# Optimization experiments

Measured on AMD Instinct MI355X. Metric: run time of the kernel, lower is better.

Reference implementation:

```python
import jax, jax.numpy as jnp
import numpy as np
import math

N_HEADS = 8

def _head_dirs():
    # 8 trigrams = corners of {-1,+1}^3, L2-normalized -> each row / sqrt(3)
    t = np.array([[ (i >> 2 & 1) * 2 - 1, (i >> 1 & 1) * 2 - 1, (i & 1) * 2 - 1]
                  for i in range(8)], dtype=np.float32)
    return jnp.asarray(t / np.sqrt(3.0, dtype=np.float32))

def setup_inputs() -> dict:
    key = jax.random.key(0)
    k1, k2, k3, k4 = jax.random.split(key, 4)
    B, T, C = 2, 2048, 1024
    x = jax.random.normal(k1, (B, T, C), dtype=jnp.float32)
    w_qkv = jax.random.normal(k2, (C, 3 * C), dtype=jnp.float32) * (1.0 / math.sqrt(C))
    w_out = jax.random.normal(k3, (C, C), dtype=jnp.float32) * (1.0 / math.sqrt(C))
    head_scales = jax.random.normal(k4, (N_HEADS,), dtype=jnp.float32) * 0.1
    return {"x": x, "w_qkv": w_qkv, "w_out": w_out, "head_scales": head_scales}

def reference(x, w_qkv, w_out, head_scales):
    B, T, C = x.shape
    H = N_HEADS
    hd = C // H
    scale = 1.0 / math.sqrt(hd)
    dirs = _head_dirs()  # [H,3], fixed buffer

    qkv = (x @ w_qkv).reshape(B, T, 3, H, hd)
    q = jnp.transpose(qkv[:, :, 0], (0, 2, 1, 3))  # [B,H,T,hd]
    k = jnp.transpose(qkv[:, :, 1], (0, 2, 1, 3))
    v = jnp.transpose(qkv[:, :, 2], (0, 2, 1, 3))

    scores = jnp.einsum('bhqd,bhkd->bhqk', q, k) * scale  # [B,H,T,T]
    causal = jnp.tril(jnp.ones((T, T), dtype=bool))
    scores = jnp.where(causal[None, None], scores, -jnp.inf)

    # rank-1 geometric (trigram) bias on first 3 dims of q,k
    q_proj = jnp.einsum('bhtd,hd->bht', q[..., :3], dirs)  # [B,H,T]
    k_proj = jnp.einsum('bhtd,hd->bht', k[..., :3], dirs)
    geo = q_proj[..., :, None] * k_proj[..., None, :]       # [B,H,T,T]
    scores = scores + head_scales[None, :, None, None] * geo

    attn = jax.nn.softmax(scores, axis=-1)
    out = jnp.einsum('bhqk,bhkd->bqhd', attn, v).reshape(B, T, C)
    return out @ w_out
```

## Files before the change

### kernel.cpp

```cpp
#include <hip/hip_runtime.h>
#include <hip/hip_bf16.h>
#include <cstdint>
#include <cstddef>


namespace {
constexpr int kB = 2, kT = 2048, kC = 1024, kHD = 128;
constexpr int kM = kB * kT;
constexpr int kN3 = 3 * kC;
constexpr float kScale = 0.08838834764831845f;
constexpr float kInvS3 = 0.57735026918962576f;
constexpr float kL2E  = 1.4426950408889634f;
}

typedef __bf16 bf16x8 __attribute__((ext_vector_type(8)));
typedef float f32x4 __attribute__((ext_vector_type(4)));
typedef unsigned short u16x8 __attribute__((ext_vector_type(8)));
typedef unsigned short u16x4 __attribute__((ext_vector_type(4)));
typedef unsigned int u32x4 __attribute__((ext_vector_type(4)));

__device__ __forceinline__ unsigned short f2b(float f) {
  return __builtin_bit_cast(unsigned short, (__bf16)f);
}
__device__ __forceinline__ float b2f(unsigned short u) {
  return (float)__builtin_bit_cast(__bf16, u);
}
__device__ __forceinline__ void gll16(const void* g, void* lds) {
  __builtin_amdgcn_global_load_lds(
      (const __attribute__((address_space(1))) unsigned int*)g,
      (__attribute__((address_space(3))) unsigned int*)lds, 16, 0, 0);
}
__device__ __forceinline__ bf16x8 ldsv(const unsigned short* p) {
  return __builtin_bit_cast(bf16x8, *(const u16x8*)p);
}

__global__ void k_cvt(const float* __restrict__ in, unsigned short* __restrict__ out, int n4) {
  int i = blockIdx.x * 256 + threadIdx.x;
  if (i >= n4) return;
  float4 v = ((const float4*)in)[i];
  u16x4 o = { f2b(v.x), f2b(v.y), f2b(v.z), f2b(v.w) };
  ((u16x4*)out)[i] = o;
}

__global__ void k_tc(const float* __restrict__ in, unsigned short* __restrict__ out,
                     int R, int Cin) {
  __shared__ float tile[64][65];
  const int t = threadIdx.x;
  const int r0 = blockIdx.y * 64, c0 = blockIdx.x * 64;
  const int tr = t >> 4, tc4 = (t & 15) * 4;
#pragma unroll
  for (int rr = 0; rr < 4; ++rr) {
    int r = tr + rr * 16;
    float4 v = *(const float4*)&in[(size_t)(r0 + r) * Cin + c0 + tc4];
    tile[r][tc4 + 0] = v.x; tile[r][tc4 + 1] = v.y;
    tile[r][tc4 + 2] = v.z; tile[r][tc4 + 3] = v.w;
  }
  __syncthreads();
#pragma unroll
  for (int rr = 0; rr < 4; ++rr) {
    int c = tr + rr * 16;
    u16x4 o = { f2b(tile[tc4 + 0][c]), f2b(tile[tc4 + 1][c]),
                f2b(tile[tc4 + 2][c]), f2b(tile[tc4 + 3][c]) };
    *(u16x4*)&out[(size_t)(c0 + c) * R + r0 + tc4] = o;
  }
}

__global__ __launch_bounds__(256, 2) void k_gemm(
    const unsigned short* __restrict__ A,
    const unsigned short* __restrict__ Bt,
    unsigned short* __restrict__ Cb,
    float* __restrict__ Cf,
    int M, int N, int K, int ldc) {
  __shared__ unsigned short sA[2][4096];
  __shared__ unsigned short sB[2][4096];
  const int t = threadIdx.x;
  const int lane = t & 63, wave = t >> 6;
  const int g = lane >> 4, c16 = lane & 15;
  const int wr = wave >> 1, wc = wave & 1;
  const int brow = blockIdx.x * 128, bcol = blockIdx.y * 128;
  const int NT = K >> 5;

  f32x4 acc[4][4];
#pragma unroll
  for (int m = 0; m < 4; ++m)
#pragma unroll
    for (int n = 0; n < 4; ++n) acc[m][n] = 0.f;

  auto stage = [&](int buf, int kt) {
    const int k0 = kt * 32;
#pragma unroll
    for (int is = 0; is < 2; ++is) {
      int row = is * 64 + (t >> 2);
      int gs = (t & 3) ^ (row & 3);
      gll16(&A[(size_t)(brow + row) * K + k0 + gs * 8], &sA[buf][is * 2048 + wave * 512]);
      gll16(&Bt[(size_t)(bcol + row) * K + k0 + gs * 8], &sB[buf][is * 2048 + wave * 512]);
    }
  };

  stage(0, 0);
  __syncthreads();
  for (int kt = 0; kt < NT; ++kt) {
    if (kt + 1 < NT) stage((kt + 1) & 1, kt + 1);
    const int buf = kt & 1;
    bf16x8 av[4], bv[4];
#pragma unroll
    for (int m = 0; m < 4; ++m) {
      int row = wr * 64 + m * 16 + c16;
      av[m] = ldsv(&sA[buf][row * 32 + (g ^ (row & 3)) * 8]);
    }
#pragma unroll
    for (int n = 0; n < 4; ++n) {
      int row = wc * 64 + n * 16 + c16;
      bv[n] = ldsv(&sB[buf][row * 32 + (g ^ (row & 3)) * 8]);
    }
    __builtin_amdgcn_s_setprio(1);
#pragma unroll
    for (int m = 0; m < 4; ++m)
#pragma unroll
      for (int n = 0; n < 4; ++n)
        acc[m][n] = __builtin_amdgcn_mfma_f32_16x16x32_bf16(av[m], bv[n], acc[m][n], 0, 0, 0);
    __builtin_amdgcn_s_setprio(0);
    __syncthreads();
  }

  const int orow = brow + wr * 64, ocol = bcol + wc * 64;
  if (Cb != nullptr) {
#pragma unroll
    for (int m = 0; m < 4; ++m)
#pragma unroll
      for (int n = 0; n < 4; ++n)
#pragma unroll
        for (int jj = 0; jj < 4; ++jj)
          Cb[(size_t)(orow + m * 16 + g * 4 + jj) * ldc + ocol + n * 16 + c16] =
              f2b(acc[m][n][jj]);
  } else {
#pragma unroll
    for (int m = 0; m < 4; ++m)
#pragma unroll
      for (int n = 0; n < 4; ++n)
#pragma unroll
        for (int jj = 0; jj < 4; ++jj)
          Cf[(size_t)(orow + m * 16 + g * 4 + jj) * ldc + ocol + n * 16 + c16] =
              acc[m][n][jj];
  }
}

__constant__ unsigned char kItem[44] = {
  60, 61,
  62, 56, 57, 58, 52,
  53, 54, 48, 49,
  50, 44, 45, 46, 40,
  41, 42, 36, 37,
  38, 32, 33, 34, 28,
  29, 30, 24, 25,
  26, 20, 21, 22, 16,
  17, 18, 12, 13, 8, 9,
  14, 4, 5, 0 };

__global__ __launch_bounds__(256, 2) void k_attn(
    const unsigned short* __restrict__ qkv,
    const float* __restrict__ head_scales,
    unsigned short* __restrict__ pO0,
    unsigned short* __restrict__ pO1,
    unsigned short* __restrict__ pO2,
    float2* __restrict__ pml) {
  __shared__ unsigned short sK[2][8192];
  __shared__ unsigned short sVt[2][128 * 72];
  __shared__ float sKp[2][64];

  const int t = threadIdx.x;
  const int lane = t & 63, wave = t >> 6;
  const int g = lane >> 4, c16 = lane & 15;
  const int bh = blockIdx.x;
  const int it = kItem[blockIdx.y];
  const int qt = it >> 2, c = it & 3;
  const int n = 2 * qt + 2;
  const int nc = (qt == 0) ? 1 : (qt <= 2) ? 2 : 3;
  const int cbase = n / nc, crem = n % nc;
  const int t0 = c * cbase + (c < crem ? c : crem);
  const int t1 = t0 + cbase + (c < crem ? 1 : 0);

  const int b = bh >> 3, h = bh & 7;
  const float hs = head_scales[h];
  const float sx = (h & 4) ? 1.f : -1.f;
  const float sy = (h & 2) ? 1.f : -1.f;
  const float sz = (h & 1) ? 1.f : -1.f;

  const int q0w = qt * 128 + wave * 32;
  const size_t rowbase = (size_t)b * kT;

  bf16x8 aq[2][4];
  float qp[2];
#pragma unroll
  for (int m = 0; m < 2; ++m) {
    const unsigned short* qrow = &qkv[(rowbase + q0w + m * 16 + c16) * kN3 + h * kHD];
#pragma unroll
    for (int ks = 0; ks < 4; ++ks) aq[m][ks] = ldsv(qrow + ks * 32 + g * 8);
    qp[m] = hs * kInvS3 * (sx * b2f(qrow[0]) + sy * b2f(qrow[1]) + sz * b2f(qrow[2]));
  }

  float mrow[2] = { -__builtin_inff(), -__builtin_inff() };
  float lrow[2] = { 0.f, 0.f };
  f32x4 oacc[2][8];
#pragma unroll
  for (int m = 0; m < 2; ++m)
#pragma unroll
    for (int dn = 0; dn < 8; ++dn) oacc[m][dn] = 0.f;

  uint4 vr[4];
  uint2 kpr;

  auto stageK = [&](int jt, int buf) {
    const int j0 = jt * 64;
#pragma unroll
    for (int is = 0; is < 4; ++is) {
      int row = is * 16 + (t >> 4);
      int gp = t & 15;
      int gs = (gp & 8) | ((gp ^ (row & 7)) & 7);
      gll16(&qkv[(rowbase + j0 + row) * kN3 + kC + h * kHD + gs * 8],
            &sK[buf][is * 2048 + wave * 512]);
    }
  };
  auto loadV = [&](int jt) {
#pragma unroll
    for (int itr = 0; itr < 4; ++itr)
      vr[itr] = *(const uint4*)&qkv[(rowbase + jt * 64 + lane) * kN3 + 2 * kC + h * kHD
                                    + (itr * 4 + wave) * 8];
  };
  auto writeV = [&](int buf) {
    unsigned int* sVtw = (unsigned int*)&sVt[buf][0];
    const int odd = lane & 1, pr = lane >> 1;
#pragma unroll
    for (int itr = 0; itr < 4; ++itr) {
      const int dg = itr * 4 + wave;
      uint4 my = vr[itr];
      unsigned int nx = __shfl_xor(my.x, 1), ny = __shfl_xor(my.y, 1);
      unsigned int nz = __shfl_xor(my.z, 1), nw = __shfl_xor(my.w, 1);
      unsigned int m01 = odd ? my.z : my.x, m23 = odd ? my.w : my.y;
      unsigned int n01 = odd ? nz : nx,     n23 = odd ? nw : ny;
      const int eb = odd * 4;
      unsigned int me, ne, w;
      me = m01 & 0xffffu;  ne = n01 & 0xffffu;
      w = odd ? (ne | (me << 16)) : (me | (ne << 16));
      sVtw[(dg * 8 + eb + 0) * 36 + pr] = w;
      me = m01 >> 16;      ne = n01 >> 16;
      w = odd ? (ne | (me << 16)) : (me | (ne << 16));
      sVtw[(dg * 8 + eb + 1) * 36 + pr] = w;
      me = m23 & 0xffffu;  ne = n23 & 0xffffu;
      w = odd ? (ne | (me << 16)) : (me | (ne << 16));
      sVtw[(dg * 8 + eb + 2) * 36 + pr] = w;
      me = m23 >> 16;      ne = n23 >> 16;
      w = odd ? (ne | (me << 16)) : (me | (ne << 16));
      sVtw[(dg * 8 + eb + 3) * 36 + pr] = w;
    }
  };
  auto loadKp = [&](int jt) {
    if (wave == 0)
      kpr = *(const uint2*)&qkv[(rowbase + jt * 64 + lane) * kN3 + kC + h * kHD];
  };
  auto writeKp = [&](int buf) {
    if (wave == 0) {
      float e0 = b2f((unsigned short)(kpr.x & 0xffffu));
      float e1 = b2f((unsigned short)(kpr.x >> 16));
      float e2 = b2f((unsigned short)(kpr.y & 0xffffu));
      sKp[buf][lane] = kInvS3 * (sx * e0 + sy * e1 + sz * e2);
    }
  };

  stageK(t0, 0); loadV(t0); loadKp(t0);
  writeV(0); writeKp(0);
  __syncthreads();

  for (int jt = t0; jt < t1; ++jt) {
    const int buf = (jt - t0) & 1;
    const bool more = (jt + 1 < t1);
    if (more) { stageK(jt + 1, buf ^ 1); loadV(jt + 1); loadKp(jt + 1); }

    const int j0 = jt * 64;
    f32x4 s[2][4];
#pragma unroll
    for (int m = 0; m < 2; ++m)
#pragma unroll
      for (int nn = 0; nn < 4; ++nn) s[m][nn] = 0.f;
#pragma unroll
    for (int ks = 0; ks < 4; ++ks) {
      bf16x8 kb[4];
#pragma unroll
      for (int nn = 0; nn < 4; ++nn) {
        int gp = ks * 4 + g;
        int gp2 = (gp & 8) | ((gp ^ (c16 & 7)) & 7);
        kb[nn] = ldsv(&sK[buf][(nn * 16 + c16) * 128 + gp2 * 8]);
      }
      __builtin_amdgcn_s_setprio(1);
#pragma unroll
      for (int m = 0; m < 2; ++m)
#pragma unroll
        for (int nn = 0; nn < 4; ++nn)
          s[m][nn] = __builtin_amdgcn_mfma_f32_16x16x32_bf16(kb[nn], aq[m][ks], s[m][nn], 0, 0, 0);
      __builtin_amdgcn_s_setprio(0);
    }

    float kpv[4][4];
#pragma unroll
    for (int nn = 0; nn < 4; ++nn)
#pragma unroll
      for (int jj = 0; jj < 4; ++jj) kpv[nn][jj] = sKp[buf][nn * 16 + g * 4 + jj];

    const bool edge = (jt >= 2 * qt);
    unsigned int paf[2][2][4];
#pragma unroll
    for (int m = 0; m < 2; ++m) {
      const int qg = q0w + m * 16 + c16;
      float vmax = -__builtin_inff();
#pragma unroll
      for (int nn = 0; nn < 4; ++nn)
#pragma unroll
        for (int jj = 0; jj < 4; ++jj) {
          float xv = s[m][nn][jj] * kScale + qp[m] * kpv[nn][jj];
          if (edge) {
            int kvg = j0 + nn * 16 + g * 4 + jj;
            xv = (kvg <= qg) ? xv : -__builtin_inff();
          }
          s[m][nn][jj] = xv;
          vmax = fmaxf(vmax, xv);
        }
      vmax = fmaxf(vmax, __shfl_xor(vmax, 16, 64));
      vmax = fmaxf(vmax, __shfl_xor(vmax, 32, 64));

      if (__any(vmax > mrow[m] + 8.f)) {
        float mnew = fmaxf(mrow[m], vmax);
        float mc0 = fmaxf(mnew, -1e30f);
        float alpha = exp2f((mrow[m] - mc0) * kL2E);
        mrow[m] = mnew;
        lrow[m] *= alpha;
        float ao[4];
#pragma unroll
        for (int jj = 0; jj < 4; ++jj)
          ao[jj] = __shfl(alpha, (lane & 48) | (g * 4 + jj), 64);
#pragma unroll
        for (int dn = 0; dn < 8; ++dn)
#pragma unroll
          for (int jj = 0; jj < 4; ++jj) oacc[m][dn][jj] *= ao[jj];
      }

      unsigned int pk[4][2];
      {
        const float mc = fmaxf(mrow[m], -1e30f);
        float ls = 0.f;
#pragma unroll
        for (int nn = 0; nn < 4; ++nn) {
          float p0 = exp2f((s[m][nn][0] - mc) * kL2E);
          float p1 = exp2f((s[m][nn][1] - mc) * kL2E);
          float p2 = exp2f((s[m][nn][2] - mc) * kL2E);
          float p3 = exp2f((s[m][nn][3] - mc) * kL2E);
          ls += (p0 + p1) + (p2 + p3);
          pk[nn][0] = (unsigned)f2b(p0) | ((unsigned)f2b(p1) << 16);
          pk[nn][1] = (unsigned)f2b(p2) | ((unsigned)f2b(p3) << 16);
        }
        lrow[m] += ls;
      }
#pragma unroll
      for (int ks2 = 0; ks2 < 2; ++ks2)
#pragma unroll
        for (int w = 0; w < 4; ++w) {
          int src = c16 + (((lane >> 4) & 1) * 2 + (w >> 1)) * 16;
          int va  = __shfl((int)pk[2 * ks2][w & 1], src, 64);
          int vb_ = __shfl((int)pk[2 * ks2 + 1][w & 1], src, 64);
          paf[m][ks2][w] = (unsigned)((lane & 32) ? vb_ : va);
        }
    }

#pragma unroll
    for (int ks2 = 0; ks2 < 2; ++ks2) {
      bf16x8 pa0 = __builtin_bit_cast(bf16x8,
          (u32x4){paf[0][ks2][0], paf[0][ks2][1], paf[0][ks2][2], paf[0][ks2][3]});
      bf16x8 pa1 = __builtin_bit_cast(bf16x8,
          (u32x4){paf[1][ks2][0], paf[1][ks2][1], paf[1][ks2][2], paf[1][ks2][3]});
      __builtin_amdgcn_s_setprio(1);
#pragma unroll
      for (int dn = 0; dn < 8; ++dn) {
        bf16x8 vb = ldsv(&sVt[buf][(dn * 16 + c16) * 72 + ks2 * 32 + g * 8]);
        oacc[0][dn] = __builtin_amdgcn_mfma_f32_16x16x32_bf16(pa0, vb, oacc[0][dn], 0, 0, 0);
        oacc[1][dn] = __builtin_amdgcn_mfma_f32_16x16x32_bf16(pa1, vb, oacc[1][dn], 0, 0, 0);
      }
      __builtin_amdgcn_s_setprio(0);
    }

    if (more) { writeV(buf ^ 1); writeKp(buf ^ 1); }
    __syncthreads();
  }

  unsigned short* pout = (c == 0) ? pO0 : (c == 1) ? pO1 : pO2;
#pragma unroll
  for (int m = 0; m < 2; ++m) {
    float lt = lrow[m];
    lt += __shfl_xor(lt, 16, 64);
    lt += __shfl_xor(lt, 32, 64);
    if (g == 0) {
      int rowi = wave * 32 + m * 16 + c16;
      pml[c * 32768 + (bh * 16 + qt) * 128 + rowi] = make_float2(mrow[m], lt);
    }
#pragma unroll
    for (int dn = 0; dn < 8; ++dn)
#pragma unroll
      for (int jj = 0; jj < 4; ++jj) {
        int r = q0w + m * 16 + g * 4 + jj;
        pout[(rowbase + r) * kC + h * kHD + dn * 16 + c16] = f2b(oacc[m][dn][jj]);
      }
  }
}

__global__ void k_comb(unsigned short* __restrict__ p0,
                       const unsigned short* __restrict__ p1,
                       const unsigned short* __restrict__ p2,
                       const float2* __restrict__ pml) {
  const int bh = blockIdx.x, qt = blockIdx.y;
  const int t = threadIdx.x;
  const int row = t >> 1, half = t & 1;
  const int b = bh >> 3, h = bh & 7;
  const size_t base = ((size_t)b * kT + qt * 128 + row) * kC + h * kHD + half * 64;
  const int nc = (qt == 0) ? 1 : (qt <= 2) ? 2 : 3;
  const int mli = (bh * 16 + qt) * 128 + row;
  float2 ml0 = pml[mli];
  float2 ml1 = make_float2(-1e30f, 0.f), ml2 = make_float2(-1e30f, 0.f);
  float mm = ml0.x;
  if (nc > 1) { ml1 = pml[32768 + mli]; mm = fmaxf(mm, ml1.x); }
  if (nc > 2) { ml2 = pml[65536 + mli]; mm = fmaxf(mm, ml2.x); }
  const float w0 = exp2f((ml0.x - mm) * kL2E);
  const float w1 = (nc > 1) ? exp2f((ml1.x - mm) * kL2E) : 0.f;
  const float w2 = (nc > 2) ? exp2f((ml2.x - mm) * kL2E) : 0.f;
  const float inv = 1.0f / (w0 * ml0.y + w1 * ml1.y + w2 * ml2.y);
#pragma unroll
  for (int i = 0; i < 8; ++i) {
    u16x8 o0 = *(const u16x8*)&p0[base + i * 8];
    u16x8 r;
    if (nc == 1) {
#pragma unroll
      for (int j = 0; j < 8; ++j) r[j] = f2b(b2f(o0[j]) * inv);
    } else if (nc == 2) {
      u16x8 o1 = *(const u16x8*)&p1[base + i * 8];
#pragma unroll
      for (int j = 0; j < 8; ++j)
        r[j] = f2b((w0 * b2f(o0[j]) + w1 * b2f(o1[j])) * inv);
    } else {
      u16x8 o1 = *(const u16x8*)&p1[base + i * 8];
      u16x8 o2 = *(const u16x8*)&p2[base + i * 8];
#pragma unroll
      for (int j = 0; j < 8; ++j)
        r[j] = f2b((w0 * b2f(o0[j]) + w1 * b2f(o1[j]) + w2 * b2f(o2[j])) * inv);
    }
    *(u16x8*)&p0[base + i * 8] = r;
  }
}

extern "C" void kernel_launch(void* const* d_in, const int* in_sizes, int n_in,
                              void* d_out, int out_size, void* d_ws, size_t ws_size,
                              hipStream_t stream) {
  const float* x    = (const float*)d_in[0];
  const float* wqkv = (const float*)d_in[1];
  const float* wout = (const float*)d_in[2];
  const float* hsc  = (const float*)d_in[3];
  char* ws = (char*)d_ws;
  unsigned short* xb    = (unsigned short*)(ws);
  unsigned short* wqkvT = (unsigned short*)(ws + 8388608);
  unsigned short* qkvb  = (unsigned short*)(ws + 16777216);
  unsigned short* attnb = (unsigned short*)(ws + 41943040);
  unsigned short* woutT = (unsigned short*)(ws);
  float2* pml = (float2*)d_out;
  float* out = (float*)d_out;

  k_cvt<<<dim3(4096), dim3(256), 0, stream>>>(x, xb, kM * kC / 4);
  k_tc<<<dim3(48, 16), dim3(256), 0, stream>>>(wqkv, wqkvT, kC, kN3);
  k_gemm<<<dim3(32, 24), dim3(256), 0, stream>>>(xb, wqkvT, qkvb, nullptr, kM, kN3, kC, kN3);
  k_attn<<<dim3(16, 44), dim3(256), 0, stream>>>(qkvb, hsc, attnb, xb, wqkvT, pml);
  k_comb<<<dim3(16, 16), dim3(256), 0, stream>>>(attnb, xb, wqkvT, pml);
  k_tc<<<dim3(16, 16), dim3(256), 0, stream>>>(wout, woutT, kC, kC);
  k_gemm<<<dim3(32, 8), dim3(256), 0, stream>>>(attnb, woutT, nullptr, out, kM, kC, kC, kC);
}
```

Baseline: 141.0 us.

## Stage V via direct global-to-LDS loads and read with transposing LDS loads

Replaces the register-staged V tile (global load, shuffle-based transpose, scattered LDS writes) with direct global_load_lds copies into a row-major V buffer. The PV MFMA operand is then fetched with ds_read_b64_tr_b16, which transposes on read. This removes the shuffles, selects and per-element LDS stores from the V path and frees the vr registers. In exchange it adds an explicit lgkmcnt wait and a scheduling barrier before the MFMAs, and correctness depends on the new LDS layout matching what the transpose read expects.

```diff
diff --git a/kernel.cpp b/kernel.cpp
--- a/kernel.cpp
+++ b/kernel.cpp
@@ -32,6 +32,12 @@
 }
 __device__ __forceinline__ bf16x8 ldsv(const unsigned short* p) {
   return __builtin_bit_cast(bf16x8, *(const u16x8*)p);
+}
+__device__ __forceinline__ uint2 tr16(const unsigned short* p) {
+  uint2 r;
+  unsigned off = (unsigned)(uintptr_t)(const __attribute__((address_space(3))) unsigned short*)p;
+  asm volatile("ds_read_b64_tr_b16 %0, %1" : "=v"(r) : "v"(off));
+  return r;
 }
 
 __global__ void k_cvt(const float* __restrict__ in, unsigned short* __restrict__ out, int n4) {
@@ -165,7 +171,7 @@
     unsigned short* __restrict__ pO2,
     float2* __restrict__ pml) {
   __shared__ unsigned short sK[2][8192];
-  __shared__ unsigned short sVt[2][128 * 72];
+  __shared__ unsigned short sV[2][8192];
   __shared__ float sKp[2][64];
 
   const int t = threadIdx.x;
@@ -207,7 +213,6 @@
 #pragma unroll
     for (int dn = 0; dn < 8; ++dn) oacc[m][dn] = 0.f;
 
-  uint4 vr[4];
   uint2 kpr;
 
   auto stageK = [&](int jt, int buf) {
@@ -221,37 +226,19 @@
             &sK[buf][is * 2048 + wave * 512]);
     }
   };
-  auto loadV = [&](int jt) {
-#pragma unroll
-    for (int itr = 0; itr < 4; ++itr)
-      vr[itr] = *(const uint4*)&qkv[(rowbase + jt * 64 + lane) * kN3 + 2 * kC + h * kHD
-                                    + (itr * 4 + wave) * 8];
-  };
-  auto writeV = [&](int buf) {
-    unsigned int* sVtw = (unsigned int*)&sVt[buf][0];
-    const int odd = lane & 1, pr = lane >> 1;
-#pragma unroll
-    for (int itr = 0; itr < 4; ++itr) {
-      const int dg = itr * 4 + wave;
-      uint4 my = vr[itr];
-      unsigned int nx = __shfl_xor(my.x, 1), ny = __shfl_xor(my.y, 1);
-      unsigned int nz = __shfl_xor(my.z, 1), nw = __shfl_xor(my.w, 1);
-      unsigned int m01 = odd ? my.z : my.x, m23 = odd ? my.w : my.y;
-      unsigned int n01 = odd ? nz : nx,     n23 = odd ? nw : ny;
-      const int eb = odd * 4;
-      unsigned int me, ne, w;
-      me = m01 & 0xffffu;  ne = n01 & 0xffffu;
-      w = odd ? (ne | (me << 16)) : (me | (ne << 16));
-      sVtw[(dg * 8 + eb + 0) * 36 + pr] = w;
-      me = m01 >> 16;      ne = n01 >> 16;
-      w = odd ? (ne | (me << 16)) : (me | (ne << 16));
-      sVtw[(dg * 8 + eb + 1) * 36 + pr] = w;
-      me = m23 & 0xffffu;  ne = n23 & 0xffffu;
-      w = odd ? (ne | (me << 16)) : (me | (ne << 16));
-      sVtw[(dg * 8 + eb + 2) * 36 + pr] = w;
-      me = m23 >> 16;      ne = n23 >> 16;
-      w = odd ? (ne | (me << 16)) : (me | (ne << 16));
-      sVtw[(dg * 8 + eb + 3) * 36 + pr] = w;
+  auto stageV = [&](int jt, int buf) {
+    const int j0 = jt * 64;
+    const int vrow = ((lane >> 3) << 2) + ((lane >> 1) & 3);
+    const int vcol = (lane & 1) * 8;
+#pragma unroll
+    for (int d = 0; d < 2; ++d) {
+      const int dn = wave * 2 + d;
+#pragma unroll
+      for (int hf2 = 0; hf2 < 2; ++hf2) {
+        gll16(&qkv[(rowbase + j0 + hf2 * 32 + vrow) * kN3 + 2 * kC + h * kHD
+                   + dn * 16 + vcol],
+              &sV[buf][dn * 1024 + hf2 * 512]);
+      }
     }
   };
   auto loadKp = [&](int jt) {
@@ -267,14 +254,14 @@
     }
   };
 
-  stageK(t0, 0); loadV(t0); loadKp(t0);
-  writeV(0); writeKp(0);
+  stageK(t0, 0); stageV(t0, 0); loadKp(t0);
+  writeKp(0);
   __syncthreads();
 
   for (int jt = t0; jt < t1; ++jt) {
     const int buf = (jt - t0) & 1;
     const bool more = (jt + 1 < t1);
-    if (more) { stageK(jt + 1, buf ^ 1); loadV(jt + 1); loadKp(jt + 1); }
+    if (more) { stageK(jt + 1, buf ^ 1); stageV(jt + 1, buf ^ 1); loadKp(jt + 1); }
 
     const int j0 = jt * 64;
     f32x4 s[2][4];
@@ -376,17 +363,26 @@
           (u32x4){paf[0][ks2][0], paf[0][ks2][1], paf[0][ks2][2], paf[0][ks2][3]});
       bf16x8 pa1 = __builtin_bit_cast(bf16x8,
           (u32x4){paf[1][ks2][0], paf[1][ks2][1], paf[1][ks2][2], paf[1][ks2][3]});
+      uint2 trv[8][2];
+#pragma unroll
+      for (int dn = 0; dn < 8; ++dn)
+#pragma unroll
+        for (int hf = 0; hf < 2; ++hf)
+          trv[dn][hf] = tr16(&sV[buf][dn * 1024 + (ks2 * 8 + 2 * g + hf) * 64 + c16 * 4]);
+      asm volatile("s_waitcnt lgkmcnt(0)" ::: "memory");
+      __builtin_amdgcn_sched_barrier(0);
       __builtin_amdgcn_s_setprio(1);
 #pragma unroll
       for (int dn = 0; dn < 8; ++dn) {
-        bf16x8 vb = ldsv(&sVt[buf][(dn * 16 + c16) * 72 + ks2 * 32 + g * 8]);
+        bf16x8 vb = __builtin_bit_cast(bf16x8,
+            (u32x4){trv[dn][0].x, trv[dn][0].y, trv[dn][1].x, trv[dn][1].y});
         oacc[0][dn] = __builtin_amdgcn_mfma_f32_16x16x32_bf16(pa0, vb, oacc[0][dn], 0, 0, 0);
         oacc[1][dn] = __builtin_amdgcn_mfma_f32_16x16x32_bf16(pa1, vb, oacc[1][dn], 0, 0, 0);
       }
       __builtin_amdgcn_s_setprio(0);
     }
 
-    if (more) { writeV(buf ^ 1); writeKp(buf ^ 1); }
+    if (more) writeKp(buf ^ 1);
     __syncthreads();
   }
 
```

After: 132.5 us. -6.0%, faster.
